# Kernel tuning notes

Hardware: AMD Instinct MI355X
Metric: run time of the kernel (lower is better)

## Reference

```python
import jax, jax.numpy as jnp
import numpy as np
from itertools import combinations

N_KERNELS, KLEN = 84, 9
MAX_IN_LENGTH, IN_CHANNELS = 512, 3
HIDDEN_DIM, MAX_DIL_PER_KERNEL = 10000, 64
BATCH = 8


def _build_params():
    """Replicates Rocket.__init__: builds the dense 'massive' conv weight and bias."""
    hd = HIDDEN_DIM // IN_CHANNELS
    nfpk = hd // N_KERNELS                      # features per kernel
    tmax = min(nfpk, MAX_DIL_PER_KERNEL)
    mult = nfpk / tmax
    max_exp = np.log2((MAX_IN_LENGTH - 1) / (KLEN - 1))
    dilations, counts = np.unique(
        np.logspace(0, max_exp, tmax, base=2).astype(np.int32), return_counts=True)
    nfpd = (counts * mult).astype(np.int32)
    rem = nfpk - int(nfpd.sum())
    i = 0
    while rem > 0:
        nfpd[i] += 1
        rem -= 1
        i = (i + 1) % len(nfpd)
    # 84 base kernels: -1 everywhere, 2 at each 3-combination of 9 positions
    W84 = np.full((N_KERNELS, KLEN), -1.0, np.float32)
    beta = np.array(list(combinations(range(KLEN), 3)), np.int32)
    W84[np.arange(len(beta))[:, None], beta] = 2.0
    maxd = int(dilations.max())
    max_pad = 4 * maxd
    out_channels = N_KERNELS * int(nfpd.sum())
    K = KLEN * maxd
    big = np.zeros((out_channels, 1, K), np.float32)
    bias_blocks = []
    i = 0
    for d, n in zip(dilations.tolist(), nfpd.tolist()):
        excess = max_pad - 4 * d
        # bias set: (n, 84), each row a constant from linspace(-1, 1, n)
        bset = np.tile(np.linspace(-1, 1, n), N_KERNELS).reshape(N_KERNELS, n).T.astype(np.float32)
        for j in range(n):
            big[(i + j) * N_KERNELS:(i + j + 1) * N_KERNELS, 0,
                excess:excess + KLEN * d:d] = W84
        bias_blocks.append(bset)
        i += n
    bias = np.concatenate(bias_blocks, 0).reshape(-1)
    return jnp.asarray(big), jnp.asarray(bias)


def setup_inputs() -> dict:
    key = jax.random.key(0)
    X = jax.random.normal(key, (BATCH, IN_CHANNELS, MAX_IN_LENGTH), dtype=jnp.float32)
    W, b = _build_params()
    return {"X": X, "W": W, "b": b}


def reference(X, W, b):
    # X: (B, C, L); W: (O, 1, K) with K = 9*max_dilation; b: (O,)
    B, C, L = X.shape
    max_pad = (W.shape[-1] // KLEN) * 4  # 4 * max_dilation
    # each channel convolved independently with the same filter bank -> fold C into batch
    x = X.reshape(B * C, 1, L)
    out = jax.lax.conv_general_dilated(
        x, W, window_strides=(1,), padding=[(max_pad, max_pad)],
        dimension_numbers=("NCH", "OIH", "NCH"))
    out = out + b[None, :, None]
    # torch cats per-channel results along dim 1 -> (B, C*O, L_out)
    return out.reshape(B, C * W.shape[0], out.shape[-1])
```

## Files before the change

kernel.cpp:

```cpp
#include <hip/hip_runtime.h>

#define LN 512
#define NK 84
#define THREADS 256

__global__ __launch_bounds__(THREADS) void rocket_fused(
    const float* __restrict__ X, const float* __restrict__ W,
    const float* __restrict__ bias, float* __restrict__ out,
    int O, int K, int T, int maxd, int max_pad, int n_groups) {
    extern __shared__ float xs[];
    __shared__ int s_d;

    const int g  = blockIdx.x % n_groups;
    const int bc = blockIdx.x / n_groups;

    if (threadIdx.x < 64) {
        const int j = threadIdx.x;
        const float* row = W + (size_t)g * NK * K;
        float v = (j <= maxd && 4 * j < K) ? row[4 * j] : 0.0f;
        unsigned long long m = __ballot(v != 0.0f);
        if (j == 0) s_d = maxd - (__ffsll(m) - 1);
    }

    for (int i = threadIdx.x; i < max_pad; i += THREADS) {
        xs[i] = 0.0f;
        xs[max_pad + LN + i] = 0.0f;
    }
    const float* xrow = X + (size_t)bc * LN;
    for (int i = threadIdx.x; i < LN; i += THREADS) {
        xs[max_pad + i] = xrow[i];
    }
    __syncthreads();

    const int   d  = s_d;
    const float bv = bias[(size_t)g * NK];
    float* const outg = out + ((size_t)bc * O + (size_t)g * NK) * T;

    const int pairs = T >> 1;
    for (int p = threadIdx.x; p < pairs; p += THREADS) {
        const int t0   = 2 * p;
        const int base = max_pad + t0 - 4 * d;
        float tx[9], ty[9];
        float s9x = 0.0f, s9y = 0.0f;
#pragma unroll
        for (int j = 0; j < 9; ++j) {
            tx[j] = xs[base + j * d];
            ty[j] = xs[base + j * d + 1];
            s9x += tx[j];
            s9y += ty[j];
        }
        const float bx = bv - s9x;
        const float by = bv - s9y;

        float* op = outg + t0;
#pragma unroll
        for (int a = 0; a < 7; ++a) {
#pragma unroll
            for (int b2 = a + 1; b2 < 8; ++b2) {
                const float px = tx[a] + tx[b2];
                const float py = ty[a] + ty[b2];
#pragma unroll
                for (int c = b2 + 1; c < 9; ++c) {
                    const float ox = fmaf(3.0f, px + tx[c], bx);
                    const float oy = fmaf(3.0f, py + ty[c], by);
                    *(float2*)op = make_float2(ox, oy);
                    op += T;
                }
            }
        }
    }

    if ((T & 1) && threadIdx.x == 0) {
        const int t    = T - 1;
        const int base = max_pad + t - 4 * d;
        float tx[9]; float s9 = 0.0f;
#pragma unroll
        for (int j = 0; j < 9; ++j) { tx[j] = xs[base + j * d]; s9 += tx[j]; }
        const float bx = bv - s9;
        float* op = outg + t;
        for (int a = 0; a < 7; ++a)
            for (int b2 = a + 1; b2 < 8; ++b2)
                for (int c = b2 + 1; c < 9; ++c) {
                    *op = fmaf(3.0f, tx[a] + tx[b2] + tx[c], bx);
                    op += T;
                }
    }
}

extern "C" void kernel_launch(void* const* d_in, const int* in_sizes, int n_in,
                              void* d_out, int out_size, void* d_ws, size_t ws_size,
                              hipStream_t stream) {
    const float* X = (const float*)d_in[0];
    const float* W = (const float*)d_in[1];
    const float* b = (const float*)d_in[2];
    float* out = (float*)d_out;

    const int O        = in_sizes[2];
    const int K        = in_sizes[1] / O;
    const int maxd     = K / 9;
    const int max_pad  = 4 * maxd;
    const int BC       = in_sizes[0] / LN;
    const int T        = out_size / (BC * O);
    const int n_groups = O / NK;

    const size_t smem = (size_t)(LN + 2 * max_pad + 4) * sizeof(float);
    rocket_fused<<<BC * n_groups, THREADS, smem, stream>>>(
        X, W, b, out, O, K, T, maxd, max_pad, n_groups);
}
```

Before: 149.2 us.

## Emit four time steps per thread with float4 stores, splitting kernel rows across halves

When T is even and fits within 126 quads, each thread now handles four consecutive output positions and writes them with float4 stores. The 84 kernel rows are split between the two 128-thread halves of the block, 42 rows each, instead of looping over pairs of positions with float2 stores. This widens stores and spreads work evenly across threads, cutting the store instruction count in this memory-bound kernel. It adds a fallback path, more register pressure, and float4 stores that may be misaligned when T is not a multiple of 4.

```diff
diff --git a/kernel.cpp b/kernel.cpp
--- a/kernel.cpp
+++ b/kernel.cpp
@@ -3,6 +3,46 @@
 #define LN 512
 #define NK 84
 #define THREADS 256
+
+
+template <int HALF>
+__device__ __forceinline__ void emit_rows(const float (&tt)[4][9],
+                                          const float (&bq)[4],
+                                          float* __restrict__ op, int T,
+                                          bool quad) {
+    constexpr int K0 = HALF * 42;
+    constexpr int K1 = K0 + 42;
+    int k = 0;
+#pragma unroll
+    for (int a = 0; a < 7; ++a) {
+#pragma unroll
+        for (int b = a + 1; b < 8; ++b) {
+            float p0 = 0.f, p1 = 0.f, p2 = 0.f, p3 = 0.f;
+            if (k + (8 - b) > K0 && k < K1) {
+                p0 = tt[0][a] + tt[0][b];
+                p1 = tt[1][a] + tt[1][b];
+                p2 = tt[2][a] + tt[2][b];
+                p3 = tt[3][a] + tt[3][b];
+            }
+#pragma unroll
+            for (int c = b + 1; c < 9; ++c) {
+                if (k >= K0 && k < K1) {
+                    const float q0 = fmaf(3.0f, p0 + tt[0][c], bq[0]);
+                    const float q1 = fmaf(3.0f, p1 + tt[1][c], bq[1]);
+                    if (quad) {
+                        const float q2 = fmaf(3.0f, p2 + tt[2][c], bq[2]);
+                        const float q3 = fmaf(3.0f, p3 + tt[3][c], bq[3]);
+                        *(float4*)op = make_float4(q0, q1, q2, q3);
+                    } else {
+                        *(float2*)op = make_float2(q0, q1);
+                    }
+                    op += T;
+                }
+                ++k;
+            }
+        }
+    }
+}
 
 __global__ __launch_bounds__(THREADS) void rocket_fused(
     const float* __restrict__ X, const float* __restrict__ W,
@@ -36,54 +76,77 @@
     const float bv = bias[(size_t)g * NK];
     float* const outg = out + ((size_t)bc * O + (size_t)g * NK) * T;
 
-    const int pairs = T >> 1;
-    for (int p = threadIdx.x; p < pairs; p += THREADS) {
-        const int t0   = 2 * p;
-        const int base = max_pad + t0 - 4 * d;
-        float tx[9], ty[9];
-        float s9x = 0.0f, s9y = 0.0f;
+    const int Q = T >> 2;
+    if ((T & 1) == 0 && Q <= 126) {
+        const int half = threadIdx.x >> 7;
+        const int i    = threadIdx.x & 127;
+        const bool quad = i < Q;
+        const bool pair = (i == Q) && ((T & 3) == 2);
+        if (quad || pair) {
+            const int t0   = 4 * i;
+            const int base = max_pad + t0 - 4 * d;
+            float tt[4][9];
+            float s0 = 0.f, s1 = 0.f, s2 = 0.f, s3 = 0.f;
 #pragma unroll
-        for (int j = 0; j < 9; ++j) {
-            tx[j] = xs[base + j * d];
-            ty[j] = xs[base + j * d + 1];
-            s9x += tx[j];
-            s9y += ty[j];
+            for (int j = 0; j < 9; ++j) {
+                const float* xp = xs + base + j * d;
+                tt[0][j] = xp[0]; tt[1][j] = xp[1];
+                tt[2][j] = xp[2]; tt[3][j] = xp[3];
+                s0 += tt[0][j]; s1 += tt[1][j];
+                s2 += tt[2][j]; s3 += tt[3][j];
+            }
+            float bq[4] = { bv - s0, bv - s1, bv - s2, bv - s3 };
+            float* op = outg + (half * 42) * T + t0;
+            if (half == 0) emit_rows<0>(tt, bq, op, T, quad);
+            else           emit_rows<1>(tt, bq, op, T, quad);
         }
-        const float bx = bv - s9x;
-        const float by = bv - s9y;
-
-        float* op = outg + t0;
+    } else {
+        const int pairs = T >> 1;
+        for (int p = threadIdx.x; p < pairs; p += THREADS) {
+            const int t0   = 2 * p;
+            const int base = max_pad + t0 - 4 * d;
+            float tx[9], ty[9];
+            float s9x = 0.0f, s9y = 0.0f;
 #pragma unroll
-        for (int a = 0; a < 7; ++a) {
+            for (int j = 0; j < 9; ++j) {
+                tx[j] = xs[base + j * d];
+                ty[j] = xs[base + j * d + 1];
+                s9x += tx[j];
+                s9y += ty[j];
+            }
+            const float bx = bv - s9x;
+            const float by = bv - s9y;
+            float* op = outg + t0;
 #pragma unroll
-            for (int b2 = a + 1; b2 < 8; ++b2) {
-                const float px = tx[a] + tx[b2];
-                const float py = ty[a] + ty[b2];
+            for (int a = 0; a < 7; ++a) {
 #pragma unroll
-                for (int c = b2 + 1; c < 9; ++c) {
-                    const float ox = fmaf(3.0f, px + tx[c], bx);
-                    const float oy = fmaf(3.0f, py + ty[c], by);
-                    *(float2*)op = make_float2(ox, oy);
-                    op += T;
+                for (int b2 = a + 1; b2 < 8; ++b2) {
+                    const float px = tx[a] + tx[b2];
+                    const float py = ty[a] + ty[b2];
+#pragma unroll
+                    for (int c = b2 + 1; c < 9; ++c) {
+                        *(float2*)op = make_float2(fmaf(3.0f, px + tx[c], bx),
+                                                   fmaf(3.0f, py + ty[c], by));
+                        op += T;
+                    }
                 }
             }
         }
-    }
-
-    if ((T & 1) && threadIdx.x == 0) {
-        const int t    = T - 1;
-        const int base = max_pad + t - 4 * d;
-        float tx[9]; float s9 = 0.0f;
+        if ((T & 1) && threadIdx.x == 0) {
+            const int t    = T - 1;
+            const int base = max_pad + t - 4 * d;
+            float tx[9]; float s9 = 0.0f;
 #pragma unroll
-        for (int j = 0; j < 9; ++j) { tx[j] = xs[base + j * d]; s9 += tx[j]; }
-        const float bx = bv - s9;
-        float* op = outg + t;
-        for (int a = 0; a < 7; ++a)
-            for (int b2 = a + 1; b2 < 8; ++b2)
-                for (int c = b2 + 1; c < 9; ++c) {
-                    *op = fmaf(3.0f, tx[a] + tx[b2] + tx[c], bx);
-                    op += T;
-                }
+            for (int j = 0; j < 9; ++j) { tx[j] = xs[base + j * d]; s9 += tx[j]; }
+            const float bx = bv - s9;
+            float* op = outg + t;
+            for (int a = 0; a < 7; ++a)
+                for (int b2 = a + 1; b2 < 8; ++b2)
+                    for (int c = b2 + 1; c < 9; ++c) {
+                        *op = fmaf(3.0f, tx[a] + tx[b2] + tx[c], bx);
+                        op += T;
+                    }
+        }
     }
 }
 
```

Measured after the change: 160.3 us. +7.4%, slower.
